# Kernel tuning notes

Measured on AMD Instinct MI355X. Metric: run time of the kernel, lower is better.

Reference implementation:

```python
import jax, jax.numpy as jnp
import numpy as np

B, NQ, NK, D, H = 4, 512, 512, 128, 32  # batch, n_queries, n_keys, kq_size, mlp hidden


def setup_inputs() -> dict:
    key = jax.random.key(0)
    ks = jax.random.split(key, 7)
    s_in = 1.0 / np.sqrt(2 * D)
    s_h = 1.0 / np.sqrt(H)
    return {
        "keys": jax.random.normal(ks[0], (B, NK, D), dtype=jnp.float32),
        "queries": jax.random.normal(ks[1], (B, NQ, D), dtype=jnp.float32),
        # first MLP layer Linear(2D, H) split into key-half and query-half
        "Wk": jax.random.uniform(ks[2], (D, H), jnp.float32, -s_in, s_in),
        "Wq": jax.random.uniform(ks[3], (D, H), jnp.float32, -s_in, s_in),
        "b1": jax.random.uniform(ks[4], (H,), jnp.float32, -s_in, s_in),
        # second MLP layer Linear(H, 1)
        "w2": jax.random.uniform(ks[5], (H,), jnp.float32, -s_h, s_h),
        "b2": jax.random.uniform(ks[6], (), jnp.float32, -s_h, s_h),
    }


def reference(keys, queries, Wk, Wq, b1, w2, b2):
    # AdditiveScorer: logits[b,q,k] = w2 . tanh(W1 @ [keys[b,k]; queries[b,q]] + b1) + b2
    # Split the concat-linear into two GEMMs (identical math, no [B,Q,K,2D] tensor).
    kh = jnp.einsum("bkd,dh->bkh", keys, Wk)            # (B, NK, H)
    qh = jnp.einsum("bqd,dh->bqh", queries, Wq)          # (B, NQ, H)
    h = jnp.tanh(qh[:, :, None, :] + kh[:, None, :, :] + b1)  # (B, NQ, NK, H)
    logits = jnp.einsum("bqkh,h->bqk", h, w2) + b2       # (B, NQ, NK)
    attn = jax.nn.softmax(logits, axis=-1)               # softmax over keys
    context = jnp.einsum("bqk,bkd->bqd", attn, keys)     # weighted value sum (values = keys)
    return context
```

## Files before the change

### kernel.cpp

```cpp
#include <hip/hip_runtime.h>

#define B 4
#define NQ 512
#define NK 512
#define D 128
#define H 32
#define G 4
#define PS 2.8853900817779268f

__device__ __forceinline__ float rcp_f(float x)  { return __builtin_amdgcn_rcpf(x); }
__device__ __forceinline__ float exp2_f(float x) { return __builtin_amdgcn_exp2f(x); }

__device__ __forceinline__ void fma4(float4& a, const float4& v, float s) {
    a.x = fmaf(s, v.x, a.x);
    a.y = fmaf(s, v.y, a.y);
    a.z = fmaf(s, v.z, a.z);
    a.w = fmaf(s, v.w, a.w);
}

__global__ __launch_bounds__(256) void proj_kernel(
    const float* __restrict__ keys, const float* __restrict__ queries,
    const float* __restrict__ Wk, const float* __restrict__ Wq,
    const float* __restrict__ b1,
    float* __restrict__ Ek, float* __restrict__ eq)
{
    __shared__ float xs[8][D];
    const int tid = threadIdx.x;
    const int r0 = blockIdx.x * 8;
    const bool is_q = (r0 >= B * NK);
    const float* __restrict__ X = is_q ? (queries + (size_t)(r0 - B * NK) * D)
                                       : (keys + (size_t)r0 * D);
    const float* __restrict__ W = is_q ? Wq : Wk;

    reinterpret_cast<float4*>(&xs[0][0])[tid] =
        reinterpret_cast<const float4*>(X)[tid];
    __syncthreads();

    const int lr = tid >> 5;
    const int h  = tid & 31;
    float a0 = 0.f, a1 = 0.f, a2 = 0.f, a3 = 0.f;
    const float4* x4 = reinterpret_cast<const float4*>(&xs[lr][0]);
    #pragma unroll
    for (int i = 0; i < D / 4; ++i) {
        float4 v = x4[i];
        a0 = fmaf(v.x, W[(4 * i + 0) * H + h], a0);
        a1 = fmaf(v.y, W[(4 * i + 1) * H + h], a1);
        a2 = fmaf(v.z, W[(4 * i + 2) * H + h], a2);
        a3 = fmaf(v.w, W[(4 * i + 3) * H + h], a3);
    }
    float acc = (a0 + a1) + (a2 + a3);
    if (is_q) {
        const int rq = r0 - B * NK + lr;
        eq[(size_t)rq * H + h] = exp2_f(acc * PS);
    } else {
        const int r = r0 + lr;
        const int b = r >> 9;
        const int k = r & (NK - 1);
        Ek[((size_t)b * H + h) * NK + k] = exp2_f((acc + b1[h]) * PS);
    }
}

__global__ __launch_bounds__(512, 6) void attend_kernel(
    const float* __restrict__ keys,
    const float* __restrict__ Ek,
    const float* __restrict__ eq,
    const float* __restrict__ w2,
    float* __restrict__ outp)
{
    __shared__ float exw[NK][G];
    __shared__ float accm[16][G][D];
    float* red = &accm[0][0][0];

    const int tid = threadIdx.x;
    const int b   = blockIdx.x >> 7;
    const int q0  = (blockIdx.x & 127) * G;

    float acc[G];
    #pragma unroll
    for (int g = 0; g < G; ++g) acc[g] = 0.f;
    const float* Ekc = Ek + (size_t)b * H * NK + tid;
    const float* eqb = eq + ((size_t)b * NQ + q0) * H;

    #pragma unroll
    for (int h4 = 0; h4 < H; h4 += 4) {
        const float ek0 = Ekc[(h4 + 0) * NK];
        const float ek1 = Ekc[(h4 + 1) * NK];
        const float ek2 = Ekc[(h4 + 2) * NK];
        const float ek3 = Ekc[(h4 + 3) * NK];
        const float w0 = w2[h4 + 0];
        const float w1 = w2[h4 + 1];
        const float wc = w2[h4 + 2];
        const float w3 = w2[h4 + 3];
        #pragma unroll
        for (int g = 0; g < G; ++g) {
            const float d0 = fmaf(eqb[g * H + h4 + 0], ek0, 1.f);
            const float d1 = fmaf(eqb[g * H + h4 + 1], ek1, 1.f);
            const float d2 = fmaf(eqb[g * H + h4 + 2], ek2, 1.f);
            const float d3 = fmaf(eqb[g * H + h4 + 3], ek3, 1.f);
            const float nab = fmaf(w1, d0, w0 * d1);
            const float ncd = fmaf(w3, d2, wc * d3);
            const float dab = d0 * d1;
            const float dcd = d2 * d3;
            const float n4  = fmaf(nab, dcd, ncd * dab);
            const float d4  = dab * dcd;
            acc[g] = fmaf(n4, rcp_f(d4), acc[g]);
        }
    }
    float e0 = exp2_f(-PS * acc[0]);
    float e1 = exp2_f(-PS * acc[1]);
    float e2 = exp2_f(-PS * acc[2]);
    float e3 = exp2_f(-PS * acc[3]);

    float s0 = e0, s1 = e1, s2 = e2, s3 = e3;
    #pragma unroll
    for (int off = 32; off; off >>= 1) {
        s0 += __shfl_xor(s0, off);
        s1 += __shfl_xor(s1, off);
        s2 += __shfl_xor(s2, off);
        s3 += __shfl_xor(s3, off);
    }
    if ((tid & 63) == 0)
        *reinterpret_cast<float4*>(red + (tid >> 6) * G) = float4{s0, s1, s2, s3};
    __syncthreads();
    float4 sum = {0.f, 0.f, 0.f, 0.f};
    #pragma unroll
    for (int p = 0; p < 8; ++p) {
        const float4 v = *reinterpret_cast<const float4*>(red + p * G);
        sum.x += v.x; sum.y += v.y; sum.z += v.z; sum.w += v.w;
    }
    *reinterpret_cast<float4*>(&exw[tid][0]) =
        float4{e0 * rcp_f(sum.x), e1 * rcp_f(sum.y),
               e2 * rcp_f(sum.z), e3 * rcp_f(sum.w)};
    __syncthreads();

    const int dg = tid & 31;
    const int kp = tid >> 5;
    const float4* k4 = reinterpret_cast<const float4*>(
        keys + ((size_t)b * NK + kp * 32) * D) + dg;
    float4 a0 = {0,0,0,0}, a1 = a0, a2 = a0, a3 = a0;
    #pragma unroll 8
    for (int kk = 0; kk < 32; ++kk) {
        const float4 ev = *reinterpret_cast<const float4*>(&exw[kp * 32 + kk][0]);
        const float4 kv = k4[(size_t)kk * (D / 4)];
        fma4(a0, kv, ev.x);
        fma4(a1, kv, ev.y);
        fma4(a2, kv, ev.z);
        fma4(a3, kv, ev.w);
    }
    *reinterpret_cast<float4*>(&accm[kp][0][4 * dg]) = a0;
    *reinterpret_cast<float4*>(&accm[kp][1][4 * dg]) = a1;
    *reinterpret_cast<float4*>(&accm[kp][2][4 * dg]) = a2;
    *reinterpret_cast<float4*>(&accm[kp][3][4 * dg]) = a3;
    __syncthreads();

    const int g = tid >> 7;
    const int d = tid & 127;
    float r = 0.f;
    #pragma unroll
    for (int p = 0; p < 16; ++p) r += accm[p][g][d];
    outp[((size_t)b * NQ + q0 + g) * D + d] = r;
}

extern "C" void kernel_launch(void* const* d_in, const int* in_sizes, int n_in,
                              void* d_out, int out_size, void* d_ws, size_t ws_size,
                              hipStream_t stream) {
    const float* keys    = (const float*)d_in[0];
    const float* queries = (const float*)d_in[1];
    const float* Wk      = (const float*)d_in[2];
    const float* Wq      = (const float*)d_in[3];
    const float* b1      = (const float*)d_in[4];
    const float* w2      = (const float*)d_in[5];
    float* out = (float*)d_out;

    float* Ek = (float*)d_ws;
    float* eq = Ek + (size_t)B * H * NK;

    const int proj_blocks = (B * NK + B * NQ) / 8;
    proj_kernel<<<proj_blocks, 256, 0, stream>>>(keys, queries, Wk, Wq, b1, Ek, eq);
    attend_kernel<<<B * NQ / G, 512, 0, stream>>>(keys, Ek, eq, w2, out);
}
```

Baseline: 20.84 us.

## Fuse projection and attend kernels with a grid-wide atomic barrier

```diff
diff --git a/kernel.cpp b/kernel.cpp
--- a/kernel.cpp
+++ b/kernel.cpp
@@ -7,6 +7,7 @@
 #define H 32
 #define G 4
 #define PS 2.8853900817779268f
+#define NBLOCKS 512
 
 __device__ __forceinline__ float rcp_f(float x)  { return __builtin_amdgcn_rcpf(x); }
 __device__ __forceinline__ float exp2_f(float x) { return __builtin_amdgcn_exp2f(x); }
@@ -18,62 +19,75 @@
     a.w = fmaf(s, v.w, a.w);
 }
 
-__global__ __launch_bounds__(256) void proj_kernel(
+__global__ __launch_bounds__(512, 6) void fused_kernel(
     const float* __restrict__ keys, const float* __restrict__ queries,
     const float* __restrict__ Wk, const float* __restrict__ Wq,
-    const float* __restrict__ b1,
-    float* __restrict__ Ek, float* __restrict__ eq)
-{
-    __shared__ float xs[8][D];
-    const int tid = threadIdx.x;
-    const int r0 = blockIdx.x * 8;
-    const bool is_q = (r0 >= B * NK);
-    const float* __restrict__ X = is_q ? (queries + (size_t)(r0 - B * NK) * D)
-                                       : (keys + (size_t)r0 * D);
-    const float* __restrict__ W = is_q ? Wq : Wk;
-
-    reinterpret_cast<float4*>(&xs[0][0])[tid] =
-        reinterpret_cast<const float4*>(X)[tid];
-    __syncthreads();
-
-    const int lr = tid >> 5;
-    const int h  = tid & 31;
-    float a0 = 0.f, a1 = 0.f, a2 = 0.f, a3 = 0.f;
-    const float4* x4 = reinterpret_cast<const float4*>(&xs[lr][0]);
-    #pragma unroll
-    for (int i = 0; i < D / 4; ++i) {
-        float4 v = x4[i];
-        a0 = fmaf(v.x, W[(4 * i + 0) * H + h], a0);
-        a1 = fmaf(v.y, W[(4 * i + 1) * H + h], a1);
-        a2 = fmaf(v.z, W[(4 * i + 2) * H + h], a2);
-        a3 = fmaf(v.w, W[(4 * i + 3) * H + h], a3);
-    }
-    float acc = (a0 + a1) + (a2 + a3);
-    if (is_q) {
-        const int rq = r0 - B * NK + lr;
-        eq[(size_t)rq * H + h] = exp2_f(acc * PS);
-    } else {
-        const int r = r0 + lr;
-        const int b = r >> 9;
-        const int k = r & (NK - 1);
-        Ek[((size_t)b * H + h) * NK + k] = exp2_f((acc + b1[h]) * PS);
-    }
-}
-
-__global__ __launch_bounds__(512, 6) void attend_kernel(
-    const float* __restrict__ keys,
-    const float* __restrict__ Ek,
-    const float* __restrict__ eq,
-    const float* __restrict__ w2,
+    const float* __restrict__ b1, const float* __restrict__ w2,
+    float* __restrict__ Ek,
+    float* __restrict__ eq,
+    unsigned int* __restrict__ ctr,
     float* __restrict__ outp)
 {
     __shared__ float exw[NK][G];
     __shared__ float accm[16][G][D];
+    float* xs  = &accm[0][0][0];
     float* red = &accm[0][0][0];
 
     const int tid = threadIdx.x;
-    const int b   = blockIdx.x >> 7;
-    const int q0  = (blockIdx.x & 127) * G;
+    const int bid = blockIdx.x;
+
+    {
+        const int r0 = bid * 8;
+        const bool is_q = (r0 >= B * NK);
+        const float* __restrict__ X = is_q ? (queries + (size_t)(r0 - B * NK) * D)
+                                           : (keys + (size_t)r0 * D);
+        const float* __restrict__ W = is_q ? Wq : Wk;
+        if (tid < 256)
+            reinterpret_cast<float4*>(xs)[tid] = reinterpret_cast<const float4*>(X)[tid];
+        __syncthreads();
+
+        const int task = tid >> 1;
+        const int half = tid & 1;
+        const int lr = task >> 5;
+        const int h  = task & 31;
+        float a0 = 0.f, a1 = 0.f, a2 = 0.f, a3 = 0.f;
+        const float4* x4 = reinterpret_cast<const float4*>(xs + lr * D) + half * 16;
+        const float* Wb = W + (half * 64) * H + h;
+        #pragma unroll
+        for (int i = 0; i < 16; ++i) {
+            float4 v = x4[i];
+            a0 = fmaf(v.x, Wb[(4 * i + 0) * H], a0);
+            a1 = fmaf(v.y, Wb[(4 * i + 1) * H], a1);
+            a2 = fmaf(v.z, Wb[(4 * i + 2) * H], a2);
+            a3 = fmaf(v.w, Wb[(4 * i + 3) * H], a3);
+        }
+        float acc = (a0 + a1) + (a2 + a3);
+        acc += __shfl_xor(acc, 1);
+        if (half == 0) {
+            if (is_q) {
+                const int rq = r0 - B * NK + lr;
+                eq[(size_t)rq * H + h] = exp2_f(acc * PS);
+            } else {
+                const int r  = r0 + lr;
+                const int bb = r >> 9;
+                const int k  = r & (NK - 1);
+                Ek[((size_t)bb * H + h) * NK + k] = exp2_f((acc + b1[h]) * PS);
+            }
+        }
+    }
+    __syncthreads();
+
+    if (tid == 0) {
+        __threadfence();
+        __hip_atomic_fetch_add(ctr, 1u, __ATOMIC_RELAXED, __HIP_MEMORY_SCOPE_AGENT);
+        while (__hip_atomic_load(ctr, __ATOMIC_RELAXED, __HIP_MEMORY_SCOPE_AGENT) < NBLOCKS)
+            __builtin_amdgcn_s_sleep(1);
+        __threadfence();
+    }
+    __syncthreads();
+
+    const int b  = bid >> 7;
+    const int q0 = (bid & 127) * G;
 
     float acc[G];
     #pragma unroll
@@ -174,8 +188,9 @@
 
     float* Ek = (float*)d_ws;
     float* eq = Ek + (size_t)B * H * NK;
+    unsigned int* ctr = (unsigned int*)(eq + (size_t)B * NQ * H);
 
-    const int proj_blocks = (B * NK + B * NQ) / 8;
-    proj_kernel<<<proj_blocks, 256, 0, stream>>>(keys, queries, Wk, Wq, b1, Ek, eq);
-    attend_kernel<<<B * NQ / G, 512, 0, stream>>>(keys, Ek, eq, w2, out);
+    hipMemsetAsync(ctr, 0, sizeof(unsigned int), stream);
+    fused_kernel<<<NBLOCKS, 512, 0, stream>>>(keys, queries, Wk, Wq, b1, w2,
+                                              Ek, eq, ctr, out);
 }
```

New measurement: 69.46 us. 3.33x slower.
